# Kernel optimization log

Measured on AMD Instinct MI355X. Metric: run time of the kernel, lower is better.

Reference implementation:

```python
import jax, jax.numpy as jnp
import numpy as np

H, FF, E = 1024, 4096, 8
CAP_FACTOR, MIN_CAP = 1.0, 4
B, S = 4, 2048


def setup_inputs() -> dict:
    key = jax.random.key(0)
    ks = jax.random.split(key, 8)
    g = lambda k, shape, sc: jax.random.normal(k, shape, jnp.float32) * sc
    return {
        "hidden_states": jax.random.normal(ks[0], (B, S, H), jnp.float32),
        "wg": g(ks[1], (H, E), 0.02),
        "w1": g(ks[2], (E, H, FF), 0.02),
        "w2": g(ks[3], (E, FF, H), 0.02),
        "res_w1": g(ks[4], (H, FF), 0.02),
        "res_w2": g(ks[5], (FF, H), 0.02),
        "coef_w": g(ks[6], (H, 2), 0.02),
        "coef_b": jnp.zeros((2,), jnp.float32),
    }


def reference(hidden_states, wg, w1, w2, res_w1, res_w2, coef_w, coef_b):
    x = hidden_states
    b, s, d = x.shape
    tokens = x.reshape(-1, d)                      # [s, m] flattened tokens
    n = tokens.shape[0]
    capacity = max(MIN_CAP, int(CAP_FACTOR * n / E))  # static

    # ---- TopKGate (top-1, deterministic, no RTS) ----
    logits = tokens @ wg                            # [s, e]
    gates = jax.nn.softmax(logits, axis=1)
    idx1 = jnp.argmax(gates, axis=1)                # [s]
    mask1 = jax.nn.one_hot(idx1, E, dtype=jnp.int32)  # [s, e]
    exp_counts = mask1.sum(axis=0)                  # [e]
    # load-balancing aux loss (computed pre-capacity-drop, as in DeepSpeed)
    me = gates.mean(axis=0)
    ce = mask1.astype(gates.dtype).mean(axis=0)
    l_aux = jnp.sum(me * ce) * E
    # capacity-based token dropping (position within expert's buffer)
    locations1 = jnp.cumsum(mask1, axis=0) - 1      # [s, e]
    mask1 = mask1 * (locations1 < capacity).astype(jnp.int32)
    loc1_s = jnp.sum(locations1 * mask1, axis=1)    # [s]
    mask1f = mask1.astype(gates.dtype)
    gates_masked = gates * mask1f                   # zero except kept expert
    loc_sc = jax.nn.one_hot(loc1_s, capacity, dtype=gates.dtype)  # [s, c]
    combine = jnp.einsum("se,sc->sec", gates_masked, loc_sc)      # [s, e, c]
    dispatch = (combine > 0).astype(tokens.dtype)                 # [s, e, c]

    # ---- dispatch -> grouped expert FFN -> combine ----
    dispatched = jnp.einsum("sec,sm->ecm", dispatch, tokens)      # [e, c, m]
    h = jax.nn.gelu(jnp.einsum("ecm,emf->ecf", dispatched, w1))
    expert_out = jnp.einsum("ecf,efm->ecm", h, w2)                # [e, c, m]
    moe_out = jnp.einsum("sec,ecm->sm", combine, expert_out).reshape(b, s, d)

    # ---- residual MoE blend ----
    res = jax.nn.gelu(x @ res_w1) @ res_w2
    coef = jax.nn.softmax(x @ coef_w + coef_b, axis=-1)           # [b, s, 2]
    out = moe_out * coef[..., 0:1] + res * coef[..., 1:2]
    return out, l_aux, exp_counts
```

## Files before the change

kernel.cpp:

```cpp
#include <hip/hip_runtime.h>

typedef unsigned short u16;
typedef unsigned int u32;
typedef float f32x4 __attribute__((ext_vector_type(4)));
typedef __bf16 bf16x8 __attribute__((ext_vector_type(8)));

#define NTOK 8192
#define HDIM 1024
#define FFDIM 4096
#define NEXP 8
#define CAP 1024

typedef const __attribute__((address_space(1))) void gvoid_t;
typedef __attribute__((address_space(3))) void lvoid_t;

__device__ __forceinline__ u16 f2bf(float f) {
  u32 u = __float_as_uint(f);
  u += 0x7fffu + ((u >> 16) & 1u);
  return (u16)(u >> 16);
}

__device__ __forceinline__ float gelu_f(float x) {
  float u = 1.5957691216057308f * (x + 0.044715f * x * x * x);
  return x / (1.0f + __expf(-u));
}

__global__ __launch_bounds__(256) void convert_bf16(const float* __restrict__ src,
                                                    u16* __restrict__ dst,
                                                    long long n) {
  long long i = ((long long)blockIdx.x * 256 + threadIdx.x) * 8;
  if (i >= n) return;
  float4 f0 = *(const float4*)(src + i);
  float4 f1 = *(const float4*)(src + i + 4);
  union { u16 u[8]; uint4 v; } o;
  o.u[0] = f2bf(f0.x); o.u[1] = f2bf(f0.y); o.u[2] = f2bf(f0.z); o.u[3] = f2bf(f0.w);
  o.u[4] = f2bf(f1.x); o.u[5] = f2bf(f1.y); o.u[6] = f2bf(f1.z); o.u[7] = f2bf(f1.w);
  *(uint4*)(dst + i) = o.v;
}

__global__ __launch_bounds__(256) void transpose_f32_bf16(const float* __restrict__ src,
                                                          long long sBatch,
                                                          u16* __restrict__ dst,
                                                          long long dBatch,
                                                          int R, int C) {
  __shared__ float tile[32][33];
  int z = blockIdx.z;
  const float* s = src + (long long)z * sBatch;
  u16* d = dst + (long long)z * dBatch;
  int c0 = blockIdx.x * 32, r0 = blockIdx.y * 32;
  int tx = threadIdx.x, ty = threadIdx.y;
#pragma unroll
  for (int i = 0; i < 32; i += 8)
    tile[ty + i][tx] = s[(long long)(r0 + ty + i) * C + c0 + tx];
  __syncthreads();
#pragma unroll
  for (int i = 0; i < 32; i += 8)
    d[(long long)(c0 + ty + i) * R + r0 + tx] = f2bf(tile[tx][ty + i]);
}

__global__ __launch_bounds__(256) void gate_kernel(const float* __restrict__ x,
                                                   const float* __restrict__ wg,
                                                   const float* __restrict__ cw,
                                                   const float* __restrict__ cb,
                                                   int* __restrict__ idx1,
                                                   float* __restrict__ gate_val,
                                                   float* __restrict__ gates8,
                                                   float* __restrict__ coef) {
  const int wave = threadIdx.x >> 6, lane = threadIdx.x & 63;
  const int s = blockIdx.x * 4 + wave;
  const float* xr = x + (long long)s * HDIM;
  double p[10];
#pragma unroll
  for (int v = 0; v < 10; ++v) p[v] = 0.0;
#pragma unroll 4
  for (int i = 0; i < HDIM / 64; ++i) {
    int hh = i * 64 + lane;
    float xv = xr[hh];
    float4 w0 = *(const float4*)(wg + hh * 8);
    float4 w1 = *(const float4*)(wg + hh * 8 + 4);
    float2 c = *(const float2*)(cw + hh * 2);
    double xd = (double)xv;
    p[0] += xd * (double)w0.x; p[1] += xd * (double)w0.y;
    p[2] += xd * (double)w0.z; p[3] += xd * (double)w0.w;
    p[4] += xd * (double)w1.x; p[5] += xd * (double)w1.y;
    p[6] += xd * (double)w1.z; p[7] += xd * (double)w1.w;
    p[8] += xd * (double)c.x;  p[9] += xd * (double)c.y;
  }
#pragma unroll
  for (int v = 0; v < 10; ++v)
#pragma unroll
    for (int off = 32; off > 0; off >>= 1) p[v] += __shfl_down(p[v], off);
  if (lane == 0) {
    double mx = p[0]; int am = 0;
#pragma unroll
    for (int e = 1; e < 8; ++e)
      if (p[e] > mx) { mx = p[e]; am = e; }
    float g[8]; float sum = 0.f;
#pragma unroll
    for (int e = 0; e < 8; ++e) { g[e] = __expf((float)(p[e] - mx)); sum += g[e]; }
    float inv = 1.f / sum;
#pragma unroll
    for (int e = 0; e < 8; ++e) { g[e] *= inv; gates8[s * 8 + e] = g[e]; }
    idx1[s] = am;
    gate_val[s] = g[am];
    float c0 = (float)p[8] + cb[0], c1 = (float)p[9] + cb[1];
    float m2 = fmaxf(c0, c1);
    float e0 = __expf(c0 - m2), e1 = __expf(c1 - m2);
    float is = 1.f / (e0 + e1);
    coef[2 * s] = e0 * is;
    coef[2 * s + 1] = e1 * is;
  }
}

__global__ void scan_kernel(const int* __restrict__ idx1,
                            const float* __restrict__ gates8,
                            int* __restrict__ rowmap,
                            float* __restrict__ out_tail)
{
  int lane = threadIdx.x;
  int cnt[8];
  float me[8];
#pragma unroll
  for (int e = 0; e < 8; ++e) { cnt[e] = 0; me[e] = 0.f; }
  unsigned long long below = (lane == 0) ? 0ull : ((~0ull) >> (64 - lane));
  int eN = idx1[lane];
  float4 gN0 = *(const float4*)(gates8 + lane * 8);
  float4 gN1 = *(const float4*)(gates8 + lane * 8 + 4);
  for (int it = 0; it < NTOK / 64; ++it) {
    int tok = it * 64 + lane;
    int e = eN;
    float4 g0 = gN0, g1 = gN1;
    if (it + 1 < NTOK / 64) {
      eN = idx1[tok + 64];
      gN0 = *(const float4*)(gates8 + (tok + 64) * 8);
      gN1 = *(const float4*)(gates8 + (tok + 64) * 8 + 4);
    }
    me[0] += g0.x; me[1] += g0.y; me[2] += g0.z; me[3] += g0.w;
    me[4] += g1.x; me[5] += g1.y; me[6] += g1.z; me[7] += g1.w;
#pragma unroll
    for (int xx = 0; xx < 8; ++xx) {
      unsigned long long m = __ballot(e == xx);
      if (e == xx) {
        int pos = cnt[xx] + __popcll(m & below);
        if (pos < CAP) rowmap[xx * CAP + pos] = tok;
      }
      cnt[xx] += __popcll(m);
    }
  }
#pragma unroll
  for (int xx = 0; xx < 8; ++xx)
#pragma unroll
    for (int off = 32; off > 0; off >>= 1) me[xx] += __shfl_down(me[xx], off);
  if (lane == 0) {
    float laux = 0.f;
#pragma unroll
    for (int e = 0; e < 8; ++e) {
      out_tail[1 + e] = (float)cnt[e];
      laux += (me[e] / (float)NTOK) * ((float)cnt[e] / (float)NTOK);
    }
    out_tail[0] = laux * (float)NEXP;
  }
}

__global__ __launch_bounds__(256) void gemm128(
    const u16* __restrict__ Aall, long long aBatch,
    const u16* __restrict__ Ball, long long bBatch,
    int M, int N, int K,
    const int* __restrict__ amapAll,
    int mode,
    u16* __restrict__ hOut, long long hBatch,
    const int* __restrict__ rmapAll,
    const float* __restrict__ gate_val,
    float* __restrict__ moe_acc,
    const float* __restrict__ coef,
    float* __restrict__ outf) {
  const int z = blockIdx.z;
  const u16* A = Aall + (long long)z * aBatch;
  const u16* Bt = Ball + (long long)z * bBatch;

  const int tid = threadIdx.x;
  const int lane = tid & 63;
  const int wave = tid >> 6;
  const int wr = wave >> 1, wc = wave & 1;
  const int tileM = blockIdx.y * 128;
  const int tileN = blockIdx.x * 128;

  __shared__ __align__(16) u16 As[128 * 64];
  __shared__ __align__(16) u16 Bs[128 * 64];

  const int lrow = lane >> 3;
  const int gk = (((lane & 7) ^ lrow) << 3);

  int sr[4];
#pragma unroll
  for (int c = 0; c < 4; ++c) sr[c] = wave * 32 + c * 8 + lrow;

  long long gaA[4];
  if (amapAll) {
    const int* amap = amapAll + (long long)z * M;
#pragma unroll
    for (int c = 0; c < 4; ++c) {
      int s0 = amap[tileM + sr[c]];
      gaA[c] = s0 < 0 ? 0 : s0;
    }
  } else {
#pragma unroll
    for (int c = 0; c < 4; ++c) gaA[c] = tileM + sr[c];
  }

  const u16* aG[4];
  const u16* bG[4];
#pragma unroll
  for (int c = 0; c < 4; ++c) {
    aG[c] = A + gaA[c] * K + gk;
    bG[c] = Bt + (long long)(tileN + sr[c]) * K + gk;
  }

  f32x4 acc[4][4];
  const f32x4 fz = {0.f, 0.f, 0.f, 0.f};
#pragma unroll
  for (int i = 0; i < 4; ++i)
#pragma unroll
    for (int j = 0; j < 4; ++j) acc[i][j] = fz;

  const int rlo = lane & 15;
  const int kq = lane >> 4;
  const int sw = rlo & 7;
  const int ks0 = (kq ^ sw) << 3;
  const int ks1 = ((4 | kq) ^ sw) << 3;
  int aRow[4], bRow[4];
#pragma unroll
  for (int i = 0; i < 4; ++i) {
    aRow[i] = (wr * 64 + i * 16 + rlo) * 64;
    bRow[i] = (wc * 64 + i * 16 + rlo) * 64;
  }

  for (int kk = 0; kk < K; kk += 64) {
    __syncthreads();
#pragma unroll
    for (int c = 0; c < 4; ++c) {
      __builtin_amdgcn_global_load_lds((gvoid_t*)aG[c],
          (lvoid_t*)&As[(wave * 32 + c * 8) * 64], 16, 0, 0);
      __builtin_amdgcn_global_load_lds((gvoid_t*)bG[c],
          (lvoid_t*)&Bs[(wave * 32 + c * 8) * 64], 16, 0, 0);
      aG[c] += 64;
      bG[c] += 64;
    }
    __syncthreads();
#pragma unroll
    for (int sub = 0; sub < 2; ++sub) {
      const int ks = sub ? ks1 : ks0;
      bf16x8 af[4], bfr[4];
#pragma unroll
      for (int i = 0; i < 4; ++i) af[i] = *(const bf16x8*)(&As[aRow[i] + ks]);
#pragma unroll
      for (int j = 0; j < 4; ++j) bfr[j] = *(const bf16x8*)(&Bs[bRow[j] + ks]);
#pragma unroll
      for (int i = 0; i < 4; ++i)
#pragma unroll
        for (int j = 0; j < 4; ++j)
          acc[i][j] = __builtin_amdgcn_mfma_f32_16x16x32_bf16(af[i], bfr[j], acc[i][j], 0, 0, 0);
    }
  }

  const int qr = (lane >> 4) * 4;
  const int cc = lane & 15;
  if (mode == 0) {
    u16* hO = hOut + (long long)z * hBatch;
#pragma unroll
    for (int i = 0; i < 4; ++i) {
      int rbase = tileM + wr * 64 + i * 16 + qr;
#pragma unroll
      for (int j = 0; j < 4; ++j) {
        int col = tileN + wc * 64 + j * 16 + cc;
#pragma unroll
        for (int r = 0; r < 4; ++r)
          hO[(long long)(rbase + r) * N + col] = f2bf(gelu_f(acc[i][j][r]));
      }
    }
  } else if (mode == 1) {
    const int* rmap = rmapAll + (long long)z * M;
#pragma unroll
    for (int i = 0; i < 4; ++i) {
      int rbase = tileM + wr * 64 + i * 16 + qr;
#pragma unroll
      for (int j = 0; j < 4; ++j) {
        int col = tileN + wc * 64 + j * 16 + cc;
#pragma unroll
        for (int r = 0; r < 4; ++r) {
          int s = rmap[rbase + r];
          if (s >= 0) moe_acc[(long long)s * HDIM + col] = gate_val[s] * acc[i][j][r];
        }
      }
    }
  } else {
#pragma unroll
    for (int i = 0; i < 4; ++i) {
      int rbase = tileM + wr * 64 + i * 16 + qr;
#pragma unroll
      for (int j = 0; j < 4; ++j) {
        int col = tileN + wc * 64 + j * 16 + cc;
#pragma unroll
        for (int r = 0; r < 4; ++r) {
          int s = rbase + r;
          outf[(long long)s * HDIM + col] =
              coef[2 * s] * moe_acc[(long long)s * HDIM + col] + coef[2 * s + 1] * acc[i][j][r];
        }
      }
    }
  }
}

extern "C" void kernel_launch(void* const* d_in, const int* in_sizes, int n_in,
                              void* d_out, int out_size, void* d_ws, size_t ws_size,
                              hipStream_t stream) {
  (void)in_sizes; (void)n_in; (void)out_size; (void)ws_size;
  const float* x   = (const float*)d_in[0];
  const float* wg  = (const float*)d_in[1];
  const float* w1  = (const float*)d_in[2];
  const float* w2  = (const float*)d_in[3];
  const float* rw1 = (const float*)d_in[4];
  const float* rw2 = (const float*)d_in[5];
  const float* cw  = (const float*)d_in[6];
  const float* cb  = (const float*)d_in[7];
  float* out = (float*)d_out;

  char* ws = (char*)d_ws;
  constexpr size_t OFF_XB   = 0;
  constexpr size_t OFF_W1T  = OFF_XB  + (size_t)NTOK * HDIM * 2;
  constexpr size_t OFF_W2T  = OFF_W1T + (size_t)NEXP * FFDIM * HDIM * 2;
  constexpr size_t OFF_H    = OFF_W2T + (size_t)NEXP * HDIM * FFDIM * 2;
  constexpr size_t OFF_MOE  = OFF_H   + (size_t)NEXP * CAP * FFDIM * 2;
  constexpr size_t OFF_GATE = OFF_MOE + (size_t)NTOK * HDIM * 4;
  constexpr size_t OFF_COEF = OFF_GATE + (size_t)NTOK * 4;
  constexpr size_t OFF_IDX  = OFF_COEF + (size_t)NTOK * 8;
  constexpr size_t OFF_RMAP = OFF_IDX + (size_t)NTOK * 4;
  constexpr size_t OFF_G8   = OFF_RMAP + (size_t)NEXP * CAP * 4;

  u16* xb        = (u16*)(ws + OFF_XB);
  u16* w1t       = (u16*)(ws + OFF_W1T);
  u16* w2t       = (u16*)(ws + OFF_W2T);
  u16* h         = (u16*)(ws + OFF_H);
  float* moe_acc = (float*)(ws + OFF_MOE);
  float* gate_v  = (float*)(ws + OFF_GATE);
  float* coef    = (float*)(ws + OFF_COEF);
  int* idx1      = (int*)(ws + OFF_IDX);
  int* rowmap    = (int*)(ws + OFF_RMAP);
  float* gates8  = (float*)(ws + OFF_G8);

  hipMemsetAsync(rowmap, 0xFF, (size_t)NEXP * CAP * 4, stream);
  hipMemsetAsync(moe_acc, 0, (size_t)NTOK * HDIM * 4, stream);

  convert_bf16<<<4096, 256, 0, stream>>>(x, xb, (long long)NTOK * HDIM);
  gate_kernel<<<NTOK / 4, 256, 0, stream>>>(x, wg, cw, cb, idx1, gate_v, gates8, coef);
  scan_kernel<<<1, 64, 0, stream>>>(idx1, gates8, rowmap, out + (size_t)NTOK * HDIM);

  transpose_f32_bf16<<<dim3(FFDIM / 32, HDIM / 32, NEXP), dim3(32, 8), 0, stream>>>(
      w1, (long long)HDIM * FFDIM, w1t, (long long)FFDIM * HDIM, HDIM, FFDIM);
  transpose_f32_bf16<<<dim3(HDIM / 32, FFDIM / 32, NEXP), dim3(32, 8), 0, stream>>>(
      w2, (long long)FFDIM * HDIM, w2t, (long long)HDIM * FFDIM, FFDIM, HDIM);

  gemm128<<<dim3(FFDIM / 128, CAP / 128, NEXP), 256, 0, stream>>>(
      xb, 0, w1t, (long long)FFDIM * HDIM, CAP, FFDIM, HDIM,
      rowmap, 0, h, (long long)CAP * FFDIM, nullptr, nullptr, nullptr, nullptr, nullptr);
  gemm128<<<dim3(HDIM / 128, CAP / 128, NEXP), 256, 0, stream>>>(
      h, (long long)CAP * FFDIM, w2t, (long long)HDIM * FFDIM, CAP, HDIM, FFDIM,
      nullptr, 1, nullptr, 0, rowmap, gate_v, moe_acc, nullptr, nullptr);

  transpose_f32_bf16<<<dim3(FFDIM / 32, HDIM / 32, 1), dim3(32, 8), 0, stream>>>(
      rw1, 0, w1t, 0, HDIM, FFDIM);
  transpose_f32_bf16<<<dim3(HDIM / 32, FFDIM / 32, 1), dim3(32, 8), 0, stream>>>(
      rw2, 0, w2t, 0, FFDIM, HDIM);

  gemm128<<<dim3(FFDIM / 128, NTOK / 128, 1), 256, 0, stream>>>(
      xb, 0, w1t, 0, NTOK, FFDIM, HDIM,
      nullptr, 0, h, 0, nullptr, nullptr, nullptr, nullptr, nullptr);
  gemm128<<<dim3(HDIM / 128, NTOK / 128, 1), 256, 0, stream>>>(
      h, 0, w2t, 0, NTOK, HDIM, FFDIM,
      nullptr, 2, nullptr, 0, nullptr, nullptr, moe_acc, coef, out);
}
```

Before: 897.4 us.

## Double-buffer GEMM LDS tiles, fold MoE blend into epilogue, merge transposes

Switches the GEMM main loop to two LDS buffers so the next K tile's global-to-LDS load is issued before the current tile's MFMAs, leaving one barrier per iteration. Reorders the work so the residual FFN runs first and writes coef1*res into the output. The expert down-projection then adds coef0*gate*acc into that output directly, which removes the fp32 moe_acc buffer, its memset and its read-back. The residual weight transposes are folded into the expert transpose launches as an extra z slice. LDS use per block doubles, which may lower occupancy.

```diff
diff --git a/kernel.cpp b/kernel.cpp
--- a/kernel.cpp
+++ b/kernel.cpp
@@ -38,14 +38,15 @@
   *(uint4*)(dst + i) = o.v;
 }
 
-__global__ __launch_bounds__(256) void transpose_f32_bf16(const float* __restrict__ src,
+__global__ __launch_bounds__(256) void transpose_f32_bf16(const float* __restrict__ srcE,
                                                           long long sBatch,
+                                                          const float* __restrict__ srcR,
                                                           u16* __restrict__ dst,
                                                           long long dBatch,
                                                           int R, int C) {
   __shared__ float tile[32][33];
   int z = blockIdx.z;
-  const float* s = src + (long long)z * sBatch;
+  const float* s = (z == NEXP) ? srcR : (srcE + (long long)z * sBatch);
   u16* d = dst + (long long)z * dBatch;
   int c0 = blockIdx.x * 32, r0 = blockIdx.y * 32;
   int tx = threadIdx.x, ty = threadIdx.y;
@@ -171,7 +172,6 @@
     u16* __restrict__ hOut, long long hBatch,
     const int* __restrict__ rmapAll,
     const float* __restrict__ gate_val,
-    float* __restrict__ moe_acc,
     const float* __restrict__ coef,
     float* __restrict__ outf) {
   const int z = blockIdx.z;
@@ -185,8 +185,8 @@
   const int tileM = blockIdx.y * 128;
   const int tileN = blockIdx.x * 128;
 
-  __shared__ __align__(16) u16 As[128 * 64];
-  __shared__ __align__(16) u16 Bs[128 * 64];
+  __shared__ __align__(16) u16 As[2][128 * 64];
+  __shared__ __align__(16) u16 Bs[2][128 * 64];
 
   const int lrow = lane >> 3;
   const int gk = (((lane & 7) ^ lrow) << 3);
@@ -235,32 +235,47 @@
     bRow[i] = (wc * 64 + i * 16 + rlo) * 64;
   }
 
+#pragma unroll
+  for (int c = 0; c < 4; ++c) {
+    __builtin_amdgcn_global_load_lds((gvoid_t*)aG[c],
+        (lvoid_t*)&As[0][(wave * 32 + c * 8) * 64], 16, 0, 0);
+    __builtin_amdgcn_global_load_lds((gvoid_t*)bG[c],
+        (lvoid_t*)&Bs[0][(wave * 32 + c * 8) * 64], 16, 0, 0);
+    aG[c] += 64;
+    bG[c] += 64;
+  }
+  __syncthreads();
+
+  int cur = 0;
   for (int kk = 0; kk < K; kk += 64) {
-    __syncthreads();
-#pragma unroll
-    for (int c = 0; c < 4; ++c) {
-      __builtin_amdgcn_global_load_lds((gvoid_t*)aG[c],
-          (lvoid_t*)&As[(wave * 32 + c * 8) * 64], 16, 0, 0);
-      __builtin_amdgcn_global_load_lds((gvoid_t*)bG[c],
-          (lvoid_t*)&Bs[(wave * 32 + c * 8) * 64], 16, 0, 0);
-      aG[c] += 64;
-      bG[c] += 64;
-    }
-    __syncthreads();
+    if (kk + 64 < K) {
+      const int nb = cur ^ 1;
+#pragma unroll
+      for (int c = 0; c < 4; ++c) {
+        __builtin_amdgcn_global_load_lds((gvoid_t*)aG[c],
+            (lvoid_t*)&As[nb][(wave * 32 + c * 8) * 64], 16, 0, 0);
+        __builtin_amdgcn_global_load_lds((gvoid_t*)bG[c],
+            (lvoid_t*)&Bs[nb][(wave * 32 + c * 8) * 64], 16, 0, 0);
+        aG[c] += 64;
+        bG[c] += 64;
+      }
+    }
 #pragma unroll
     for (int sub = 0; sub < 2; ++sub) {
       const int ks = sub ? ks1 : ks0;
       bf16x8 af[4], bfr[4];
 #pragma unroll
-      for (int i = 0; i < 4; ++i) af[i] = *(const bf16x8*)(&As[aRow[i] + ks]);
-#pragma unroll
-      for (int j = 0; j < 4; ++j) bfr[j] = *(const bf16x8*)(&Bs[bRow[j] + ks]);
+      for (int i = 0; i < 4; ++i) af[i] = *(const bf16x8*)(&As[cur][aRow[i] + ks]);
+#pragma unroll
+      for (int j = 0; j < 4; ++j) bfr[j] = *(const bf16x8*)(&Bs[cur][bRow[j] + ks]);
 #pragma unroll
       for (int i = 0; i < 4; ++i)
 #pragma unroll
         for (int j = 0; j < 4; ++j)
           acc[i][j] = __builtin_amdgcn_mfma_f32_16x16x32_bf16(af[i], bfr[j], acc[i][j], 0, 0, 0);
     }
+    __syncthreads();
+    cur ^= 1;
   }
 
   const int qr = (lane >> 4) * 4;
@@ -289,7 +304,10 @@
 #pragma unroll
         for (int r = 0; r < 4; ++r) {
           int s = rmap[rbase + r];
-          if (s >= 0) moe_acc[(long long)s * HDIM + col] = gate_val[s] * acc[i][j][r];
+          if (s >= 0) {
+            long long o = (long long)s * HDIM + col;
+            outf[o] = coef[2 * s] * gate_val[s] * acc[i][j][r] + outf[o];
+          }
         }
       }
     }
@@ -303,8 +321,7 @@
 #pragma unroll
         for (int r = 0; r < 4; ++r) {
           int s = rbase + r;
-          outf[(long long)s * HDIM + col] =
-              coef[2 * s] * moe_acc[(long long)s * HDIM + col] + coef[2 * s + 1] * acc[i][j][r];
+          outf[(long long)s * HDIM + col] = coef[2 * s + 1] * acc[i][j][r];
         }
       }
     }
@@ -328,10 +345,9 @@
   char* ws = (char*)d_ws;
   constexpr size_t OFF_XB   = 0;
   constexpr size_t OFF_W1T  = OFF_XB  + (size_t)NTOK * HDIM * 2;
-  constexpr size_t OFF_W2T  = OFF_W1T + (size_t)NEXP * FFDIM * HDIM * 2;
-  constexpr size_t OFF_H    = OFF_W2T + (size_t)NEXP * HDIM * FFDIM * 2;
-  constexpr size_t OFF_MOE  = OFF_H   + (size_t)NEXP * CAP * FFDIM * 2;
-  constexpr size_t OFF_GATE = OFF_MOE + (size_t)NTOK * HDIM * 4;
+  constexpr size_t OFF_W2T  = OFF_W1T + (size_t)(NEXP + 1) * FFDIM * HDIM * 2;
+  constexpr size_t OFF_H    = OFF_W2T + (size_t)(NEXP + 1) * HDIM * FFDIM * 2;
+  constexpr size_t OFF_GATE = OFF_H   + (size_t)NTOK * FFDIM * 2;
   constexpr size_t OFF_COEF = OFF_GATE + (size_t)NTOK * 4;
   constexpr size_t OFF_IDX  = OFF_COEF + (size_t)NTOK * 8;
   constexpr size_t OFF_RMAP = OFF_IDX + (size_t)NTOK * 4;
@@ -341,7 +357,6 @@
   u16* w1t       = (u16*)(ws + OFF_W1T);
   u16* w2t       = (u16*)(ws + OFF_W2T);
   u16* h         = (u16*)(ws + OFF_H);
-  float* moe_acc = (float*)(ws + OFF_MOE);
   float* gate_v  = (float*)(ws + OFF_GATE);
   float* coef    = (float*)(ws + OFF_COEF);
   int* idx1      = (int*)(ws + OFF_IDX);
@@ -349,33 +364,27 @@
   float* gates8  = (float*)(ws + OFF_G8);
 
   hipMemsetAsync(rowmap, 0xFF, (size_t)NEXP * CAP * 4, stream);
-  hipMemsetAsync(moe_acc, 0, (size_t)NTOK * HDIM * 4, stream);
 
   convert_bf16<<<4096, 256, 0, stream>>>(x, xb, (long long)NTOK * HDIM);
   gate_kernel<<<NTOK / 4, 256, 0, stream>>>(x, wg, cw, cb, idx1, gate_v, gates8, coef);
   scan_kernel<<<1, 64, 0, stream>>>(idx1, gates8, rowmap, out + (size_t)NTOK * HDIM);
 
-  transpose_f32_bf16<<<dim3(FFDIM / 32, HDIM / 32, NEXP), dim3(32, 8), 0, stream>>>(
-      w1, (long long)HDIM * FFDIM, w1t, (long long)FFDIM * HDIM, HDIM, FFDIM);
-  transpose_f32_bf16<<<dim3(HDIM / 32, FFDIM / 32, NEXP), dim3(32, 8), 0, stream>>>(
-      w2, (long long)FFDIM * HDIM, w2t, (long long)HDIM * FFDIM, FFDIM, HDIM);
+  transpose_f32_bf16<<<dim3(FFDIM / 32, HDIM / 32, NEXP + 1), dim3(32, 8), 0, stream>>>(
+      w1, (long long)HDIM * FFDIM, rw1, w1t, (long long)FFDIM * HDIM, HDIM, FFDIM);
+  transpose_f32_bf16<<<dim3(HDIM / 32, FFDIM / 32, NEXP + 1), dim3(32, 8), 0, stream>>>(
+      w2, (long long)FFDIM * HDIM, rw2, w2t, (long long)HDIM * FFDIM, FFDIM, HDIM);
+
+  gemm128<<<dim3(FFDIM / 128, NTOK / 128, 1), 256, 0, stream>>>(
+      xb, 0, w1t + (size_t)NEXP * FFDIM * HDIM, 0, NTOK, FFDIM, HDIM,
+      nullptr, 0, h, 0, nullptr, nullptr, nullptr, nullptr);
+  gemm128<<<dim3(HDIM / 128, NTOK / 128, 1), 256, 0, stream>>>(
+      h, 0, w2t + (size_t)NEXP * HDIM * FFDIM, 0, NTOK, HDIM, FFDIM,
+      nullptr, 2, nullptr, 0, nullptr, nullptr, coef, out);
 
   gemm128<<<dim3(FFDIM / 128, CAP / 128, NEXP), 256, 0, stream>>>(
       xb, 0, w1t, (long long)FFDIM * HDIM, CAP, FFDIM, HDIM,
-      rowmap, 0, h, (long long)CAP * FFDIM, nullptr, nullptr, nullptr, nullptr, nullptr);
+      rowmap, 0, h, (long long)CAP * FFDIM, nullptr, nullptr, nullptr, nullptr);
   gemm128<<<dim3(HDIM / 128, CAP / 128, NEXP), 256, 0, stream>>>(
       h, (long long)CAP * FFDIM, w2t, (long long)HDIM * FFDIM, CAP, HDIM, FFDIM,
-      nullptr, 1, nullptr, 0, rowmap, gate_v, moe_acc, nullptr, nullptr);
-
-  transpose_f32_bf16<<<dim3(FFDIM / 32, HDIM / 32, 1), dim3(32, 8), 0, stream>>>(
-      rw1, 0, w1t, 0, HDIM, FFDIM);
-  transpose_f32_bf16<<<dim3(HDIM / 32, FFDIM / 32, 1), dim3(32, 8), 0, stream>>>(
-      rw2, 0, w2t, 0, FFDIM, HDIM);
-
-  gemm128<<<dim3(FFDIM / 128, NTOK / 128, 1), 256, 0, stream>>>(
-      xb, 0, w1t, 0, NTOK, FFDIM, HDIM,
-      nullptr, 0, h, 0, nullptr, nullptr, nullptr, nullptr, nullptr);
-  gemm128<<<dim3(HDIM / 128, NTOK / 128, 1), 256, 0, stream>>>(
-      h, 0, w2t, 0, NTOK, HDIM, FFDIM,
-      nullptr, 2, nullptr, 0, nullptr, nullptr, moe_acc, coef, out);
-}
+      nullptr, 1, nullptr, 0, rowmap, gate_v, coef, out);
+}
```

After: 883.6 us. Within noise of the previous version (-1.5%).
